# Optimization experiments

Hardware: AMD Instinct MI355X
Metric: run time of the kernel (lower is better)

## Reference

```python
import jax, jax.numpy as jnp
import numpy as np

DIM = 512
NUM_HEADS = 8
HEAD_DIM = DIM // NUM_HEADS
SCALE = HEAD_DIM ** -0.5


def setup_inputs() -> dict:
    key = jax.random.key(0)
    k1, k2, k3, k4 = jax.random.split(key, 4)
    x = jax.random.normal(k1, (2, 4096, DIM), dtype=jnp.float32)
    # Linear weights stored as (in, out) for x @ W; torch Linear(dim, 3*dim, bias=False)
    w_qkv = jax.random.normal(k2, (DIM, 3 * DIM), dtype=jnp.float32) * (DIM ** -0.5)
    w_proj = jax.random.normal(k3, (DIM, DIM), dtype=jnp.float32) * (DIM ** -0.5)
    b_proj = jax.random.normal(k4, (DIM,), dtype=jnp.float32) * 0.02
    return {"x": x, "w_qkv": w_qkv, "w_proj": w_proj, "b_proj": b_proj}


def reference(x, w_qkv, w_proj, b_proj):
    B, N, C = x.shape
    qkv = (x @ w_qkv).reshape(B, N, 3, NUM_HEADS, HEAD_DIM)
    qkv = jnp.transpose(qkv, (2, 0, 3, 1, 4))  # (3, B, H, N, hd)
    q, k, v = qkv[0], qkv[1], qkv[2]
    attn = jnp.einsum("bhnd,bhmd->bhnm", q, k) * SCALE
    attn = jax.nn.softmax(attn, axis=-1)
    out = jnp.einsum("bhnm,bhmd->bhnd", attn, v)
    out = jnp.transpose(out, (0, 2, 1, 3)).reshape(B, N, C)
    return out @ w_proj + b_proj
```

## Files before the change

kernel.cpp:

```cpp
#include <hip/hip_runtime.h>
#include <hip/hip_bf16.h>
#include <stdint.h>
#include <math.h>

#define NC3 1536
#define QSCALE 0.18033688011111907f
#define KSPLIT 2

typedef __attribute__((ext_vector_type(8))) short short8;
typedef __attribute__((ext_vector_type(4))) short short4v;
typedef __attribute__((ext_vector_type(4))) float f32x4;
typedef __attribute__((ext_vector_type(16))) float f32x16;
typedef __attribute__((ext_vector_type(8))) _Float16 f16x8;
typedef __attribute__((ext_vector_type(2))) __fp16 fp16x2;

static __device__ __forceinline__ short f2bf(float f) {
    union { __hip_bfloat16 h; short s; } u;
    u.h = __float2bfloat16(f);
    return u.s;
}
static __device__ __forceinline__ float bf2f(short s) {
    return __uint_as_float(((unsigned)(unsigned short)s) << 16);
}
static __device__ __forceinline__ short f2h(float f) {
    union { __fp16 h; short s; } u;
    u.h = (__fp16)f;
    return u.s;
}
static __device__ __forceinline__ unsigned hpack(float a, float b) {
    union { fp16x2 h; unsigned u; } c;
    c.h = __builtin_amdgcn_cvt_pkrtz(a, b);
    return c.u;
}

#define GLD_LDS(g, l)                                                          \
    __builtin_amdgcn_global_load_lds(                                          \
        (const __attribute__((address_space(1))) void*)(g),                    \
        (__attribute__((address_space(3))) void*)(l), 16, 0, 0)

__global__ __launch_bounds__(256) void prep(const float* __restrict__ x,
                                            short* __restrict__ xbf,
                                            const float* __restrict__ wqkv,
                                            short* __restrict__ wqkvT,
                                            const float* __restrict__ wproj,
                                            short* __restrict__ wprojT) {
    int tx = threadIdx.x, ty = threadIdx.y;
    int tid = ty * 32 + tx;
    if (blockIdx.z == 0) {
        int bid = blockIdx.y * 48 + blockIdx.x;
        for (int i = bid * 256 + tid; i < 1048576; i += 768 * 256) {
            float4 v = ((const float4*)x)[i];
            short4v o = {f2bf(v.x), f2bf(v.y), f2bf(v.z), f2bf(v.w)};
            ((short4v*)xbf)[i] = o;
        }
        return;
    }
    const float* src;
    short* dst;
    int C;
    bool tof16;
    if (blockIdx.z == 1) { src = wqkv; dst = wqkvT; C = 1536; tof16 = false; }
    else                 { if (blockIdx.x >= 16) return; src = wproj; dst = wprojT; C = 512; tof16 = true; }
    __shared__ short t[32][33];
    int c0 = blockIdx.x * 32, r0 = blockIdx.y * 32;
#pragma unroll
    for (int i = 0; i < 4; i++) {
        float v = src[(size_t)(r0 + ty + i * 8) * C + c0 + tx];
        t[ty + i * 8][tx] = tof16 ? f2h(v) : f2bf(v);
    }
    __syncthreads();
#pragma unroll
    for (int i = 0; i < 4; i++)
        dst[(size_t)(c0 + ty + i * 8) * 512 + r0 + tx] = t[tx][ty + i * 8];
}

__global__ __launch_bounds__(256) void gemm_qkv(const short* __restrict__ A,
                                                const short* __restrict__ Bt,
                                                short* __restrict__ Out,
                                                short* __restrict__ VT) {
    __shared__ __attribute__((aligned(16))) short smem[2][128 * 64];
    short* a_sm = &smem[0][0];
    short* b_sm = &smem[1][0];
    const int tid = threadIdx.x;
    const int lane = tid & 63;
    const int wave = tid >> 6;
    const int wr = wave >> 1, wc = wave & 1;
    const int quad = lane >> 4;
    const int l15 = lane & 15;
    const int m0 = blockIdx.x * 128;
    const int n0 = blockIdx.y * 128;
    const int srow = lane >> 3;
    const int schunk = (lane & 7) ^ srow;

    f32x4 zero4 = {0.f, 0.f, 0.f, 0.f};
    f32x4 acc[4][4];
#pragma unroll
    for (int i = 0; i < 4; i++)
#pragma unroll
        for (int j = 0; j < 4; j++) acc[i][j] = zero4;

    for (int k0 = 0; k0 < 512; k0 += 64) {
        __syncthreads();
#pragma unroll
        for (int i = 0; i < 4; i++) {
            int r0 = wave * 32 + i * 8;
            GLD_LDS(A + (size_t)(m0 + r0 + srow) * 512 + k0 + schunk * 8, a_sm + r0 * 64);
            GLD_LDS(Bt + (size_t)(n0 + r0 + srow) * 512 + k0 + schunk * 8, b_sm + r0 * 64);
        }
        __syncthreads();
#pragma unroll
        for (int kk = 0; kk < 2; kk++) {
            short8 af[4], bfr[4];
#pragma unroll
            for (int mi = 0; mi < 4; mi++) {
                int row = wr * 64 + mi * 16 + l15;
                af[mi] = *(const short8*)(a_sm + row * 64 + (((kk * 4 + quad) ^ (row & 7))) * 8);
            }
#pragma unroll
            for (int ni = 0; ni < 4; ni++) {
                int row = wc * 64 + ni * 16 + l15;
                bfr[ni] = *(const short8*)(b_sm + row * 64 + (((kk * 4 + quad) ^ (row & 7))) * 8);
            }
#pragma unroll
            for (int mi = 0; mi < 4; mi++)
#pragma unroll
                for (int ni = 0; ni < 4; ni++)
                    acc[mi][ni] = __builtin_amdgcn_mfma_f32_16x16x32_bf16(
                        af[mi], bfr[ni], acc[mi][ni], 0, 0, 0);
        }
    }

#pragma unroll
    for (int mi = 0; mi < 4; mi++) {
#pragma unroll
        for (int ni = 0; ni < 4; ni++) {
            int gm0 = m0 + wr * 64 + mi * 16 + quad * 4;
            int gn = n0 + wc * 64 + ni * 16 + l15;
            f32x4 v = acc[mi][ni];
#pragma unroll
            for (int r = 0; r < 4; r++) {
                float val = v[r];
                float o = (gn < 512) ? val * QSCALE : val;
                Out[(size_t)(gm0 + r) * NC3 + gn] = f2bf(o);
            }
        }
    }

    if (n0 >= 1024) {
        __syncthreads();
        short* lt = &smem[0][0];
        const int sq = ((quad & 1) << 1) | (quad >> 1);
#pragma unroll
        for (int mi = 0; mi < 4; mi++) {
#pragma unroll
            for (int ni = 0; ni < 4; ni++) {
                int cl = wc * 64 + ni * 16 + l15;
                int tg = wr * 16 + mi * 4 + sq;
                int tg2 = tg ^ ((cl & 7) << 1);
                f32x4 v = acc[mi][ni];
                uint2 pk;
                pk.x = hpack(v[0], v[1]);
                pk.y = hpack(v[2], v[3]);
                *(uint2*)(lt + cl * 128 + tg2 * 4) = pk;
            }
        }
        __syncthreads();
        int cl = tid >> 1, half = tid & 1;
        int cv = n0 - 1024 + cl;
        int h = cv >> 6, d = cv & 63;
        int btok = m0 >> 12;
        int mt = m0 & 4095;
        short* vrow = VT + ((size_t)((btok * 8 + h) * 64 + d)) * 4096 + mt + half * 64;
        int m = (cl & 7) << 1;
#pragma unroll
        for (int j = 0; j < 8; j++) {
            int tg = half * 16 + j * 2;
            short8 v8 = *(const short8*)(lt + cl * 128 + (tg ^ m) * 4);
            *(short8*)(vrow + j * 8) = v8;
        }
    }
}

__global__ __launch_bounds__(256, 4) void attn_kernel(const short* __restrict__ QKV,
                                                      const short* __restrict__ VT,
                                                      short* __restrict__ Op0,
                                                      short* __restrict__ Op1,
                                                      float* __restrict__ lpart) {
    __shared__ __attribute__((aligned(16))) short k_sm[2][64 * 64];
    __shared__ __attribute__((aligned(16))) short v_sm[2][64 * 64];

    const int tid = threadIdx.x;
    const int lane = tid & 63;
    const int wave = tid >> 6;
    const int l31 = lane & 31;
    const int hi = lane >> 5;
    const int qt = blockIdx.x;
    const int bh = blockIdx.y;
    const int ks = blockIdx.z;
    const int b = bh >> 3, h = bh & 7;
    const size_t tokbase = (size_t)b * 4096;
    const int rowbase = qt * 128;
    const int kt0 = ks * (64 / KSPLIT);
    const int kt1 = kt0 + (64 / KSPLIT);
    const short* Qg = QKV + h * 64;
    const short* Kg = QKV + 512 + h * 64;
    const short* VTg = VT + (size_t)bh * 64 * 4096;
    const int srow = lane >> 3;
    const int schunk = (lane & 7) ^ srow;

    short* qstage = &k_sm[0][0];
#pragma unroll
    for (int i = 0; i < 4; i++) {
        int r0 = wave * 32 + i * 8;
        GLD_LDS(Qg + (tokbase + rowbase + r0 + srow) * NC3 + schunk * 8, qstage + r0 * 64);
    }
    __syncthreads();
    const int qrow = wave * 32 + l31;
    short8 qf[4];
#pragma unroll
    for (int kk = 0; kk < 4; kk++) {
        int slot = (kk * 2 + hi) ^ (qrow & 7);
        qf[kk] = *(const short8*)(qstage + qrow * 64 + slot * 8);
    }
    __syncthreads();

#pragma unroll
    for (int i = 0; i < 2; i++) {
        int r0 = wave * 16 + i * 8;
        GLD_LDS(Kg + (tokbase + (size_t)kt0 * 64 + r0 + srow) * NC3 + schunk * 8,
                k_sm[0] + r0 * 64);
        GLD_LDS(VTg + (size_t)(r0 + srow) * 4096 + kt0 * 64 + schunk * 8,
                v_sm[0] + r0 * 64);
    }

    const _Float16 onef = (_Float16)1.0f;
    const f16x8 ones16 = {onef, onef, onef, onef, onef, onef, onef, onef};

    f32x16 acc_o[2], acc_l;
#pragma unroll
    for (int i = 0; i < 16; i++) { acc_o[0][i] = 0.f; acc_o[1][i] = 0.f; acc_l[i] = 0.f; }

    for (int kt = kt0; kt < kt1; kt++) {
        __syncthreads();
        const int cur = kt & 1;
        if (kt < kt1 - 1) {
            const int nb = cur ^ 1;
#pragma unroll
            for (int i = 0; i < 2; i++) {
                int r0 = wave * 16 + i * 8;
                GLD_LDS(Kg + (tokbase + (size_t)(kt + 1) * 64 + r0 + srow) * NC3 + schunk * 8,
                        k_sm[nb] + r0 * 64);
                GLD_LDS(VTg + (size_t)(r0 + srow) * 4096 + (kt + 1) * 64 + schunk * 8,
                        v_sm[nb] + r0 * 64);
            }
        }

        f32x16 s[2];
#pragma unroll
        for (int i = 0; i < 16; i++) { s[0][i] = 0.f; s[1][i] = 0.f; }
#pragma unroll
        for (int kk = 0; kk < 4; kk++) {
#pragma unroll
            for (int kb = 0; kb < 2; kb++) {
                int row = kb * 32 + l31;
                int slot = (kk * 2 + hi) ^ (row & 7);
                short8 kf = *(const short8*)(k_sm[cur] + row * 64 + slot * 8);
                s[kb] = __builtin_amdgcn_mfma_f32_32x32x16_bf16(kf, qf[kk], s[kb], 0, 0, 0);
            }
        }

        unsigned pk[2][8];
#pragma unroll
        for (int kb = 0; kb < 2; kb++)
#pragma unroll
            for (int i = 0; i < 16; i += 2)
                pk[kb][i >> 1] = hpack(__builtin_amdgcn_exp2f(s[kb][i]),
                                       __builtin_amdgcn_exp2f(s[kb][i + 1]));

#pragma unroll
        for (int g = 0; g < 4; g++) {
            union { unsigned u[4]; f16x8 v; } pf;
#pragma unroll
            for (int t = 0; t < 4; t++) pf.u[t] = pk[g >> 1][4 * (g & 1) + t];
            acc_l = __builtin_amdgcn_mfma_f32_32x32x16_f16(ones16, pf.v, acc_l, 0, 0, 0);
#pragma unroll
            for (int db = 0; db < 2; db++) {
                int row = db * 32 + l31;
                int slot = (g * 2 + hi) ^ (row & 7);
                f16x8 vf = *(const f16x8*)(v_sm[cur] + row * 64 + slot * 8);
                acc_o[db] = __builtin_amdgcn_mfma_f32_32x32x16_f16(vf, pf.v, acc_o[db], 0, 0, 0);
            }
        }
    }

    __syncthreads();

    size_t growq = tokbase + rowbase + qrow;
    if (hi == 0) lpart[(size_t)ks * 65536 + growq * 8 + h] = acc_l[0];

    short* osm = &k_sm[0][0] + wave * 2048;
#pragma unroll
    for (int db = 0; db < 2; db++) {
#pragma unroll
        for (int i = 0; i < 16; i += 2) {
            int d = db * 32 + (i & 3) + 8 * (i >> 2) + 4 * hi;
            unsigned pkd = hpack(acc_o[db][i], acc_o[db][i + 1]);
            int slot = (d >> 3) ^ (l31 & 7);
            *(unsigned*)(osm + l31 * 64 + slot * 8 + (d & 7)) = pkd;
        }
    }
    short* Od = (ks == 0) ? Op0 : Op1;
#pragma unroll
    for (int j = 0; j < 4; j++) {
        int r = lane >> 1;
        int c = (lane & 1) * 4 + j;
        int slot = c ^ (r & 7);
        short8 ov = *(const short8*)(osm + r * 64 + slot * 8);
        size_t grow = tokbase + rowbase + wave * 32 + r;
        *(short8*)(Od + grow * 512 + h * 64 + c * 8) = ov;
    }
}

__global__ __launch_bounds__(256) void gemm_proj(const short* __restrict__ Op0,
                                                 const short* __restrict__ Op1,
                                                 const float* __restrict__ lpart,
                                                 const short* __restrict__ Bt,
                                                 float* __restrict__ OutF,
                                                 const float* __restrict__ bias) {
    __shared__ __attribute__((aligned(16))) short a0_sm[128 * 64];
    __shared__ __attribute__((aligned(16))) short a1_sm[128 * 64];
    __shared__ __attribute__((aligned(16))) short b_sm[64 * 64];
    __shared__ float linv_sm[128 * 8];
    const int tid = threadIdx.x;
    const int lane = tid & 63;
    const int wave = tid >> 6;
    const int wr = wave >> 1, wc = wave & 1;
    const int quad = lane >> 4;
    const int l15 = lane & 15;
    const int m0 = blockIdx.x * 128;
    const int n0 = blockIdx.y * 64;
    const int srow = lane >> 3;
    const int schunk = (lane & 7) ^ srow;

    {
        int idx = tid * 4;
        int row = idx >> 3;
        int hh = idx & 7;
        float4 va = *(const float4*)(lpart + (size_t)(m0 + row) * 8 + hh);
        float4 vb = *(const float4*)(lpart + 65536 + (size_t)(m0 + row) * 8 + hh);
        linv_sm[idx + 0] = 1.0f / (va.x + vb.x);
        linv_sm[idx + 1] = 1.0f / (va.y + vb.y);
        linv_sm[idx + 2] = 1.0f / (va.z + vb.z);
        linv_sm[idx + 3] = 1.0f / (va.w + vb.w);
    }

    f32x4 zero4 = {0.f, 0.f, 0.f, 0.f};
    f32x4 acc[4][2];
#pragma unroll
    for (int i = 0; i < 4; i++) { acc[i][0] = zero4; acc[i][1] = zero4; }

    for (int k0 = 0; k0 < 512; k0 += 64) {
        __syncthreads();
#pragma unroll
        for (int i = 0; i < 4; i++) {
            int r0 = wave * 32 + i * 8;
            GLD_LDS(Op0 + (size_t)(m0 + r0 + srow) * 512 + k0 + schunk * 8, a0_sm + r0 * 64);
            GLD_LDS(Op1 + (size_t)(m0 + r0 + srow) * 512 + k0 + schunk * 8, a1_sm + r0 * 64);
        }
#pragma unroll
        for (int i = 0; i < 2; i++) {
            int r0 = wave * 16 + i * 8;
            GLD_LDS(Bt + (size_t)(n0 + r0 + srow) * 512 + k0 + schunk * 8, b_sm + r0 * 64);
        }
        __syncthreads();
        const int h = k0 >> 6;
#pragma unroll
        for (int kk = 0; kk < 2; kk++) {
            f16x8 af[4], bfr[2];
#pragma unroll
            for (int mi = 0; mi < 4; mi++) {
                int row = wr * 64 + mi * 16 + l15;
                int slot = (kk * 4 + quad) ^ (row & 7);
                f16x8 a0v = *(const f16x8*)(a0_sm + row * 64 + slot * 8);
                f16x8 a1v = *(const f16x8*)(a1_sm + row * 64 + slot * 8);
                _Float16 lh = (_Float16)linv_sm[row * 8 + h];
                f16x8 lv = {lh, lh, lh, lh, lh, lh, lh, lh};
                af[mi] = (a0v + a1v) * lv;
            }
#pragma unroll
            for (int ni = 0; ni < 2; ni++) {
                int row = wc * 32 + ni * 16 + l15;
                int slot = (kk * 4 + quad) ^ (row & 7);
                bfr[ni] = *(const f16x8*)(b_sm + row * 64 + slot * 8);
            }
#pragma unroll
            for (int mi = 0; mi < 4; mi++)
#pragma unroll
                for (int ni = 0; ni < 2; ni++)
                    acc[mi][ni] = __builtin_amdgcn_mfma_f32_16x16x32_f16(
                        af[mi], bfr[ni], acc[mi][ni], 0, 0, 0);
        }
    }

#pragma unroll
    for (int mi = 0; mi < 4; mi++) {
#pragma unroll
        for (int ni = 0; ni < 2; ni++) {
            int gm0 = m0 + wr * 64 + mi * 16 + quad * 4;
            int gn = n0 + wc * 32 + ni * 16 + l15;
            f32x4 v = acc[mi][ni];
#pragma unroll
            for (int r = 0; r < 4; r++)
                OutF[(size_t)(gm0 + r) * 512 + gn] = v[r] + bias[gn];
        }
    }
}

extern "C" void kernel_launch(void* const* d_in, const int* in_sizes, int n_in,
                              void* d_out, int out_size, void* d_ws, size_t ws_size,
                              hipStream_t stream) {
    (void)in_sizes; (void)n_in; (void)out_size; (void)ws_size;
    const float* x = (const float*)d_in[0];
    const float* wqkv = (const float*)d_in[1];
    const float* wproj = (const float*)d_in[2];
    const float* bproj = (const float*)d_in[3];
    float* out = (float*)d_out;

    short* ws = (short*)d_ws;
    short* xbf = ws;
    short* wqkvT = xbf + (size_t)4194304;
    short* wprojT = wqkvT + (size_t)1536 * 512;
    short* QKV = wprojT + (size_t)512 * 512;
    short* VTb = QKV + (size_t)8192 * 1536;
    short* Op0 = VTb + (size_t)16 * 64 * 4096;
    short* Op1 = xbf;
    float* lpart = (float*)wqkvT;

    prep<<<dim3(48, 16, 3), dim3(32, 8), 0, stream>>>(x, xbf, wqkv, wqkvT, wproj, wprojT);
    gemm_qkv<<<dim3(64, 12), 256, 0, stream>>>(xbf, wqkvT, QKV, VTb);
    attn_kernel<<<dim3(32, 16, KSPLIT), 256, 0, stream>>>(QKV, VTb, Op0, Op1, lpart);
    gemm_proj<<<dim3(64, 8), 256, 0, stream>>>(Op0, Op1, lpart, wprojT, out, bproj);
}
```

Baseline: 201.5 us.

## Remap blocks across XCDs, drop ones-MFMA row sum, add setprio in attention

Remaps block indices in the QKV GEMM, the attention kernel and the projection GEMM so that each XCD gets a contiguous group of tiles sharing the same operands, aiming at better L2 reuse. In attention, the softmax denominator is now summed with scalar adds plus a cross-half shuffle, replacing the extra MFMA against a ones vector. The kernel also raises wave priority around the compute section and unrolls the K/V tile loops by hand. The remapping assumes fixed grid shapes and round-robin dispatch across 8 XCDs, and the scalar adds put more load on the VALU.

```diff
diff --git a/kernel.cpp b/kernel.cpp
--- a/kernel.cpp
+++ b/kernel.cpp
@@ -87,8 +87,11 @@
     const int wr = wave >> 1, wc = wave & 1;
     const int quad = lane >> 4;
     const int l15 = lane & 15;
-    const int m0 = blockIdx.x * 128;
-    const int n0 = blockIdx.y * 128;
+    const int orig = blockIdx.y * 64 + blockIdx.x;
+    const int xcd = orig & 7;
+    const int lid = orig >> 3;
+    const int m0 = (xcd * 8 + (lid & 7)) * 128;
+    const int n0 = (lid >> 3) * 128;
     const int srow = lane >> 3;
     const int schunk = (lane & 7) ^ srow;
 
@@ -194,14 +197,19 @@
     const int wave = tid >> 6;
     const int l31 = lane & 31;
     const int hi = lane >> 5;
-    const int qt = blockIdx.x;
-    const int bh = blockIdx.y;
-    const int ks = blockIdx.z;
+    const int orig = (blockIdx.z * 16 + blockIdx.y) * 32 + blockIdx.x;
+    const int xcd = orig & 7;
+    const int lid = orig >> 3;
+    const int qt = lid & 31;
+    const int pr = xcd * 4 + (lid >> 5);
+    const int bh = pr & 15;
+    const int ks = pr >> 4;
     const int b = bh >> 3, h = bh & 7;
     const size_t tokbase = (size_t)b * 4096;
     const int rowbase = qt * 128;
-    const int kt0 = ks * (64 / KSPLIT);
-    const int kt1 = kt0 + (64 / KSPLIT);
+    constexpr int NT = 64 / KSPLIT;
+    const int kt0 = ks * NT;
+    const int kt1 = kt0 + NT;
     const short* Qg = QKV + h * 64;
     const short* Kg = QKV + 512 + h * 64;
     const short* VTg = VT + (size_t)bh * 64 * 4096;
@@ -233,12 +241,10 @@
                 v_sm[0] + r0 * 64);
     }
 
-    const _Float16 onef = (_Float16)1.0f;
-    const f16x8 ones16 = {onef, onef, onef, onef, onef, onef, onef, onef};
-
-    f32x16 acc_o[2], acc_l;
-#pragma unroll
-    for (int i = 0; i < 16; i++) { acc_o[0][i] = 0.f; acc_o[1][i] = 0.f; acc_l[i] = 0.f; }
+    f32x16 acc_o0, acc_o1;
+#pragma unroll
+    for (int i = 0; i < 16; i++) { acc_o0[i] = 0.f; acc_o1[i] = 0.f; }
+    float la0 = 0.f, la1 = 0.f;
 
     for (int kt = kt0; kt < kt1; kt++) {
         __syncthreads();
@@ -254,60 +260,70 @@
                         v_sm[nb] + r0 * 64);
             }
         }
-
-        f32x16 s[2];
-#pragma unroll
-        for (int i = 0; i < 16; i++) { s[0][i] = 0.f; s[1][i] = 0.f; }
+        __builtin_amdgcn_s_setprio(1);
+
+        f32x16 s0, s1;
+#pragma unroll
+        for (int i = 0; i < 16; i++) { s0[i] = 0.f; s1[i] = 0.f; }
 #pragma unroll
         for (int kk = 0; kk < 4; kk++) {
-#pragma unroll
-            for (int kb = 0; kb < 2; kb++) {
-                int row = kb * 32 + l31;
-                int slot = (kk * 2 + hi) ^ (row & 7);
-                short8 kf = *(const short8*)(k_sm[cur] + row * 64 + slot * 8);
-                s[kb] = __builtin_amdgcn_mfma_f32_32x32x16_bf16(kf, qf[kk], s[kb], 0, 0, 0);
-            }
+            int slot = (kk * 2 + hi) ^ (l31 & 7);
+            short8 kf0 = *(const short8*)(k_sm[cur] + l31 * 64 + slot * 8);
+            s0 = __builtin_amdgcn_mfma_f32_32x32x16_bf16(kf0, qf[kk], s0, 0, 0, 0);
+            short8 kf1 = *(const short8*)(k_sm[cur] + (32 + l31) * 64 + slot * 8);
+            s1 = __builtin_amdgcn_mfma_f32_32x32x16_bf16(kf1, qf[kk], s1, 0, 0, 0);
         }
 
         unsigned pk[2][8];
 #pragma unroll
-        for (int kb = 0; kb < 2; kb++)
-#pragma unroll
-            for (int i = 0; i < 16; i += 2)
-                pk[kb][i >> 1] = hpack(__builtin_amdgcn_exp2f(s[kb][i]),
-                                       __builtin_amdgcn_exp2f(s[kb][i + 1]));
+        for (int t = 0; t < 16; t += 2) {
+            float e0 = __builtin_amdgcn_exp2f(s0[t]);
+            float e1 = __builtin_amdgcn_exp2f(s0[t + 1]);
+            pk[0][t >> 1] = hpack(e0, e1);
+            la0 += e0 + e1;
+        }
+#pragma unroll
+        for (int t = 0; t < 16; t += 2) {
+            float e0 = __builtin_amdgcn_exp2f(s1[t]);
+            float e1 = __builtin_amdgcn_exp2f(s1[t + 1]);
+            pk[1][t >> 1] = hpack(e0, e1);
+            la1 += e0 + e1;
+        }
 
 #pragma unroll
         for (int g = 0; g < 4; g++) {
             union { unsigned u[4]; f16x8 v; } pf;
 #pragma unroll
             for (int t = 0; t < 4; t++) pf.u[t] = pk[g >> 1][4 * (g & 1) + t];
-            acc_l = __builtin_amdgcn_mfma_f32_32x32x16_f16(ones16, pf.v, acc_l, 0, 0, 0);
-#pragma unroll
-            for (int db = 0; db < 2; db++) {
-                int row = db * 32 + l31;
-                int slot = (g * 2 + hi) ^ (row & 7);
-                f16x8 vf = *(const f16x8*)(v_sm[cur] + row * 64 + slot * 8);
-                acc_o[db] = __builtin_amdgcn_mfma_f32_32x32x16_f16(vf, pf.v, acc_o[db], 0, 0, 0);
-            }
-        }
+            {
+                int slot = (g * 2 + hi) ^ (l31 & 7);
+                f16x8 vf0 = *(const f16x8*)(v_sm[cur] + l31 * 64 + slot * 8);
+                acc_o0 = __builtin_amdgcn_mfma_f32_32x32x16_f16(vf0, pf.v, acc_o0, 0, 0, 0);
+                f16x8 vf1 = *(const f16x8*)(v_sm[cur] + (32 + l31) * 64 + slot * 8);
+                acc_o1 = __builtin_amdgcn_mfma_f32_32x32x16_f16(vf1, pf.v, acc_o1, 0, 0, 0);
+            }
+        }
+        __builtin_amdgcn_s_setprio(0);
     }
 
     __syncthreads();
 
+    float l_acc = la0 + la1;
+    l_acc += __shfl_xor(l_acc, 32);
     size_t growq = tokbase + rowbase + qrow;
-    if (hi == 0) lpart[(size_t)ks * 65536 + growq * 8 + h] = acc_l[0];
+    if (hi == 0) lpart[(size_t)ks * 65536 + growq * 8 + h] = l_acc;
 
     short* osm = &k_sm[0][0] + wave * 2048;
 #pragma unroll
-    for (int db = 0; db < 2; db++) {
-#pragma unroll
-        for (int i = 0; i < 16; i += 2) {
-            int d = db * 32 + (i & 3) + 8 * (i >> 2) + 4 * hi;
-            unsigned pkd = hpack(acc_o[db][i], acc_o[db][i + 1]);
-            int slot = (d >> 3) ^ (l31 & 7);
-            *(unsigned*)(osm + l31 * 64 + slot * 8 + (d & 7)) = pkd;
-        }
+    for (int i = 0; i < 16; i += 2) {
+        int d0 = (i & 3) + 8 * (i >> 2) + 4 * hi;
+        unsigned pkd0 = hpack(acc_o0[i], acc_o0[i + 1]);
+        int slot0 = (d0 >> 3) ^ (l31 & 7);
+        *(unsigned*)(osm + l31 * 64 + slot0 * 8 + (d0 & 7)) = pkd0;
+        int d1 = 32 + d0;
+        unsigned pkd1 = hpack(acc_o1[i], acc_o1[i + 1]);
+        int slot1 = (d1 >> 3) ^ (l31 & 7);
+        *(unsigned*)(osm + l31 * 64 + slot1 * 8 + (d1 & 7)) = pkd1;
     }
     short* Od = (ks == 0) ? Op0 : Op1;
 #pragma unroll
@@ -337,8 +353,11 @@
     const int wr = wave >> 1, wc = wave & 1;
     const int quad = lane >> 4;
     const int l15 = lane & 15;
-    const int m0 = blockIdx.x * 128;
-    const int n0 = blockIdx.y * 64;
+    const int orig = blockIdx.y * 64 + blockIdx.x;
+    const int xcd = orig & 7;
+    const int lid = orig >> 3;
+    const int m0 = (xcd * 8 + (lid & 7)) * 128;
+    const int n0 = (lid >> 3) * 64;
     const int srow = lane >> 3;
     const int schunk = (lane & 7) ^ srow;
 
```

Result: no change. 197.7 us (-1.9%).
